# Kernel tuning notes

Hardware: AMD Instinct MI355X
Metric: run time of the kernel (lower is better)

Reference implementation:

```python
import jax, jax.numpy as jnp
import numpy as np

G = 256          # grid resolution -> V = G*G vertices
B = 8            # batch of meshes
N_SAMPLES = 2048
W_CHAMFER, W_EDGE, W_NORMAL, W_LAP = 1.0, 1.0, 0.1, 0.1
V = G * G


def _grid_faces(g):
    idx = np.arange(g * g).reshape(g, g)
    v00 = idx[:-1, :-1].ravel(); v01 = idx[:-1, 1:].ravel()
    v10 = idx[1:, :-1].ravel();  v11 = idx[1:, 1:].ravel()
    f1 = np.stack([v00, v01, v10], 1)
    f2 = np.stack([v01, v11, v10], 1)
    return np.concatenate([f1, f2], 0).astype(np.int32)  # [F,3]


def _edges_and_pairs(faces, n_verts):
    # all face-edge incidences + the opposite vertex of each incidence
    e = np.concatenate([faces[:, [0, 1]], faces[:, [1, 2]], faces[:, [0, 2]]], 0)
    opp = np.concatenate([faces[:, 2], faces[:, 0], faces[:, 1]], 0)
    e = np.sort(e, 1)
    key = e[:, 0].astype(np.int64) * n_verts + e[:, 1]
    order = np.argsort(key, kind='stable')
    key_s, es, opps = key[order], e[order], opp[order]
    first = np.ones(len(key_s), bool); first[1:] = key_s[1:] != key_s[:-1]
    edges = es[first].astype(np.int32)                      # unique undirected edges [E,2]
    dup = np.nonzero(~first)[0]                             # 2nd incidence of shared edges
    pairs = np.stack([es[dup - 1, 0], es[dup - 1, 1], opps[dup - 1], opps[dup]], 1).astype(np.int32)  # [P,4]
    return edges, pairs


def setup_inputs() -> dict:
    key = jax.random.key(0)
    faces = _grid_faces(G)
    edges, nc_pairs = _edges_and_pairs(faces, V)
    # base grid geometry + gaussian perturbation (realistic smooth-ish surfaces)
    xs, ys = np.meshgrid(np.linspace(0, 1, G), np.linspace(0, 1, G), indexing='ij')
    base = np.stack([xs, ys, 0.1 * np.sin(4 * np.pi * xs) * np.cos(4 * np.pi * ys)], -1).reshape(V, 3)
    k1, k2 = jax.random.split(key)
    verts_pred = jnp.asarray(base, jnp.float32)[None] + 0.01 * jax.random.normal(k1, (B, V, 3), jnp.float32)
    verts_targ = jnp.asarray(base, jnp.float32)[None] + 0.01 * jax.random.normal(k2, (B, V, 3), jnp.float32)
    return {
        'verts_pred': verts_pred,
        'verts_targ': verts_targ,
        'faces': jnp.asarray(faces),
        'edges': jnp.asarray(edges),
        'nc_pairs': jnp.asarray(nc_pairs),
    }


def _sample_points(verts, faces, key, n):
    # verts [V,3]; area-weighted face sampling + uniform barycentric (pytorch3d scheme)
    v0, v1, v2 = verts[faces[:, 0]], verts[faces[:, 1]], verts[faces[:, 2]]
    areas = 0.5 * jnp.linalg.norm(jnp.cross(v1 - v0, v2 - v0), axis=-1)          # [F]
    kf, kb = jax.random.split(key)
    fidx = jax.random.categorical(kf, jnp.log(areas + 1e-12), shape=(n,))        # [n]
    uv = jax.random.uniform(kb, (n, 2), verts.dtype)
    su = jnp.sqrt(uv[:, 0:1]); vv = uv[:, 1:2]
    w0, w1, w2 = 1.0 - su, su * (1.0 - vv), su * vv
    return w0 * v0[fidx] + w1 * v1[fidx] + w2 * v2[fidx]                         # [n,3]


def _chamfer(x, y):
    # squared-distance chamfer, mean over points then batch, both directions summed
    d = jnp.sum((x[:, :, None, :] - y[:, None, :, :]) ** 2, -1)                  # [B,N,M]
    return jnp.mean(jnp.min(d, axis=2)) + jnp.mean(jnp.min(d, axis=1))


def _edge_loss(verts, edges):
    diff = verts[:, edges[:, 0]] - verts[:, edges[:, 1]]                          # [B,E,3]
    return jnp.mean(jnp.sum(diff * diff, -1))                                     # (||e|| - 0)^2


def _normal_consistency(verts, nc_pairs):
    v0 = verts[:, nc_pairs[:, 0]]; v1 = verts[:, nc_pairs[:, 1]]
    a = verts[:, nc_pairs[:, 2]]; b = verts[:, nc_pairs[:, 3]]
    e = v1 - v0
    n0 = jnp.cross(e, a - v0)
    n1 = -jnp.cross(e, b - v0)
    eps = 1e-8
    cos = jnp.sum(n0 * n1, -1) / (
        jnp.maximum(jnp.linalg.norm(n0, axis=-1), eps)
        * jnp.maximum(jnp.linalg.norm(n1, axis=-1), eps))
    return jnp.mean(1.0 - cos)


def _laplacian_uniform(verts, edges):
    e0, e1 = edges[:, 0], edges[:, 1]
    ones = jnp.ones((edges.shape[0],), verts.dtype)

    def per_mesh(v):  # v [V,3]
        nsum = (jax.ops.segment_sum(v[e1], e0, num_segments=V)
                + jax.ops.segment_sum(v[e0], e1, num_segments=V))
        deg = (jax.ops.segment_sum(ones, e0, num_segments=V)
               + jax.ops.segment_sum(ones, e1, num_segments=V))
        lap = nsum / jnp.maximum(deg, 1.0)[:, None] - v                           # D^-1 A v - v
        return jnp.mean(jnp.linalg.norm(lap, axis=-1))

    return jnp.mean(jax.vmap(per_mesh)(verts))


def reference(verts_pred, verts_targ, faces, edges, nc_pairs):
    skey = jax.random.key(42)
    kp = jax.random.split(jax.random.fold_in(skey, 0), verts_pred.shape[0])
    kt = jax.random.split(jax.random.fold_in(skey, 1), verts_targ.shape[0])
    sample_pred = jax.vmap(lambda v, k: _sample_points(v, faces, k, N_SAMPLES))(verts_pred, kp)
    sample_targ = jax.vmap(lambda v, k: _sample_points(v, faces, k, N_SAMPLES))(verts_targ, kt)
    loss_chamfer = _chamfer(sample_pred, sample_targ)
    loss_edge = _edge_loss(verts_pred, edges)
    loss_normal = _normal_consistency(verts_pred, nc_pairs)
    loss_lap = _laplacian_uniform(verts_pred, edges)
    loss = (W_CHAMFER * loss_chamfer + W_EDGE * loss_edge
            + W_NORMAL * loss_normal + W_LAP * loss_lap)
    return (loss, loss_chamfer, loss_edge, loss_normal, loss_lap)
```

## Files before the change

kernel.cpp:

```cpp
#include <hip/hip_runtime.h>
#include <stdint.h>

#define GSZ 256
#define NV (GSZ*GSZ)
#define NS 2048
#define CELLS (255*255)
#define FH CELLS
#define NF (2*CELLS)
#define CH 8

struct F3 { float x, y, z; };

__device__ __forceinline__ F3 ldv3(const float* __restrict__ p, int idx) {
    const float* q = p + 3*(size_t)idx;
    F3 r; r.x = q[0]; r.y = q[1]; r.z = q[2]; return r;
}
__device__ __forceinline__ F3 f3sub(F3 a, F3 b) { return F3{a.x-b.x, a.y-b.y, a.z-b.z}; }
__device__ __forceinline__ F3 f3cross(F3 a, F3 b) {
    return F3{a.y*b.z - a.z*b.y, a.z*b.x - a.x*b.z, a.x*b.y - a.y*b.x};
}
__device__ __forceinline__ float f3dot(F3 a, F3 b) { return a.x*b.x + a.y*b.y + a.z*b.z; }

__device__ __forceinline__ uint64_t splitmix64(uint64_t& s) {
    s += 0x9E3779B97F4A7C15ULL;
    uint64_t z = s;
    z = (z ^ (z >> 30)) * 0xBF58476D1CE4E5B9ULL;
    z = (z ^ (z >> 27)) * 0x94D049BB133111EBULL;
    return z ^ (z >> 31);
}

__device__ __forceinline__ float blockReduceSum256(float v) {
    __shared__ float s[4];
    int lane = threadIdx.x & 63, w = threadIdx.x >> 6;
    #pragma unroll
    for (int o = 32; o > 0; o >>= 1) v += __shfl_down(v, o, 64);
    if (lane == 0) s[w] = v;
    __syncthreads();
    if (threadIdx.x == 0) v = s[0] + s[1] + s[2] + s[3];
    return v;
}

__global__ void k_area(const float* __restrict__ vp, const float* __restrict__ vt,
                       int B, float* __restrict__ areas, float* __restrict__ blockmax,
                       unsigned* __restrict__ counter) {
    if (blockIdx.x == 0 && threadIdx.x == 0) *counter = 0u;
    int gid = blockIdx.x*256 + threadIdx.x;
    int total = 2*B*CELLS;
    float mloc = 0.f;
    if (gid < total) {
        int m = gid / CELLS;
        int c = gid - m*CELLS;
        int i = c / 255, j = c - i*255;
        const float* verts = (m < B ? vp + (size_t)m*NV*3
                                    : vt + (size_t)(m-B)*NV*3);
        int b00 = i*GSZ + j;
        F3 v00 = ldv3(verts, b00);
        F3 v01 = ldv3(verts, b00+1);
        F3 v10 = ldv3(verts, b00+GSZ);
        F3 v11 = ldv3(verts, b00+GSZ+1);
        F3 c1 = f3cross(f3sub(v01, v00), f3sub(v10, v00));
        F3 c2 = f3cross(f3sub(v11, v01), f3sub(v10, v01));
        float a1 = 0.5f * sqrtf(f3dot(c1, c1));
        float a2 = 0.5f * sqrtf(f3dot(c2, c2));
        size_t base = (size_t)m*NF;
        areas[base + c]      = a1;
        areas[base + FH + c] = a2;
        mloc = fmaxf(a1, a2);
    }
    #pragma unroll
    for (int o = 32; o > 0; o >>= 1) mloc = fmaxf(mloc, __shfl_down(mloc, o, 64));
    __shared__ float s[4];
    int lane = threadIdx.x & 63, w = threadIdx.x >> 6;
    if (lane == 0) s[w] = mloc;
    __syncthreads();
    if (threadIdx.x == 0)
        blockmax[blockIdx.x] = fmaxf(fmaxf(s[0], s[1]), fmaxf(s[2], s[3]));
}

__global__ void k_sample(const float* __restrict__ vp, const float* __restrict__ vt,
                         int B, const float* __restrict__ areas,
                         const float* __restrict__ blockmax, int nbm,
                         float4* __restrict__ samples) {
    float m = 0.f;
    for (int k = threadIdx.x; k < nbm; k += 256) m = fmaxf(m, blockmax[k]);
    #pragma unroll
    for (int o = 32; o > 0; o >>= 1) m = fmaxf(m, __shfl_down(m, o, 64));
    __shared__ float s[4];
    int lane = threadIdx.x & 63, w = threadIdx.x >> 6;
    if (lane == 0) s[w] = m;
    __syncthreads();
    __shared__ float sMaxA;
    if (threadIdx.x == 0) sMaxA = fmaxf(fmaxf(s[0], s[1]), fmaxf(s[2], s[3]));
    __syncthreads();
    float maxA = sMaxA;

    int gid = blockIdx.x*256 + threadIdx.x;
    int cloud = gid / (B*NS);
    int rem = gid - cloud*(B*NS);
    int b = rem / NS;
    const float* verts = (cloud ? vt : vp) + (size_t)b*NV*3;
    const float* am = areas + (size_t)(cloud*B + b)*NF;

    uint64_t st = ((uint64_t)(gid + 1) * 0x9E3779B97F4A7C15ULL) ^ 0xC0FFEE123456789ULL;
    int f = 0;
    for (int round = 0; round < 64; ++round) {
        uint64_t r0 = splitmix64(st), r1 = splitmix64(st);
        uint64_t r2 = splitmix64(st), r3 = splitmix64(st);
        int f0 = (int)(((uint64_t)(uint32_t)r0 * (uint32_t)NF) >> 32);
        int f1 = (int)(((uint64_t)(uint32_t)r1 * (uint32_t)NF) >> 32);
        int f2 = (int)(((uint64_t)(uint32_t)r2 * (uint32_t)NF) >> 32);
        int f3 = (int)(((uint64_t)(uint32_t)r3 * (uint32_t)NF) >> 32);
        float a0 = am[f0], a1 = am[f1], a2 = am[f2], a3 = am[f3];
        float u0 = ((uint32_t)(r0 >> 40)) * (1.f/16777216.f);
        float u1 = ((uint32_t)(r1 >> 40)) * (1.f/16777216.f);
        float u2 = ((uint32_t)(r2 >> 40)) * (1.f/16777216.f);
        float u3 = ((uint32_t)(r3 >> 40)) * (1.f/16777216.f);
        if (u0 * maxA <= a0) { f = f0; break; }
        if (u1 * maxA <= a1) { f = f1; break; }
        if (u2 * maxA <= a2) { f = f2; break; }
        if (u3 * maxA <= a3) { f = f3; break; }
        f = f3;
    }
    int i0, i1, i2;
    if (f < FH) {
        int c = f;  int i = c / 255, j = c - i*255;  int v = i*GSZ + j;
        i0 = v; i1 = v + 1; i2 = v + GSZ;
    } else {
        int c = f - FH;  int i = c / 255, j = c - i*255;  int v = i*GSZ + j;
        i0 = v + 1; i1 = v + GSZ + 1; i2 = v + GSZ;
    }
    F3 v0 = ldv3(verts, i0), v1 = ldv3(verts, i1), v2 = ldv3(verts, i2);
    uint64_t r = splitmix64(st);
    float u0 = ((uint32_t)r >> 8) * (1.f/16777216.f);
    float u1 = ((uint32_t)(r >> 32) >> 8) * (1.f/16777216.f);
    float su = sqrtf(u0);
    float w0 = 1.f - su, w1 = su * (1.f - u1), w2 = su * u1;
    float X = w0*v0.x + w1*v1.x + w2*v2.x;
    float Y = w0*v0.y + w1*v1.y + w2*v2.y;
    float Z = w0*v0.z + w1*v1.z + w2*v2.z;
    samples[gid] = make_float4(X, Y, Z, X*X + Y*Y + Z*Z);
}

__global__ void k_heavy(const float* __restrict__ vp,
                        const float4* __restrict__ samples,
                        const int* __restrict__ edges, const int* __restrict__ ncp,
                        int B, int E, int P, int nbE, int nbP,
                        float* __restrict__ minpart,
                        float* __restrict__ partE, float* __restrict__ partP,
                        float* __restrict__ partV) {
    int bx = blockIdx.x, b = blockIdx.y;
    if (bx < 64) {
        int xh = bx >> 5, z = bx & 31;
        int dir = z >> 4, q = z & 15;
        const float4* src = samples + ((size_t)dir*B + b)*NS;
        const float4* dst = samples + ((size_t)(1-dir)*B + b)*NS;

        __shared__ float4 tile[128];
        if (threadIdx.x < 128) tile[threadIdx.x] = dst[q*128 + threadIdx.x];

        float nx[4], ny[4], nz[4], xx[4], mn[4];
        #pragma unroll
        for (int k = 0; k < 4; ++k) {
            int i = xh*1024 + k*256 + threadIdx.x;
            float4 sp = src[i];
            nx[k] = -2.f*sp.x; ny[k] = -2.f*sp.y; nz[k] = -2.f*sp.z;
            xx[k] = sp.w;
            mn[k] = 3.402823466e38f;
        }
        __syncthreads();
        #pragma unroll 4
        for (int j = 0; j < 128; ++j) {
            float4 t = tile[j];
            #pragma unroll
            for (int k = 0; k < 4; ++k) {
                float d = fmaf(nx[k], t.x, t.w);
                d = fmaf(ny[k], t.y, d);
                d = fmaf(nz[k], t.z, d);
                mn[k] = fminf(mn[k], d);
            }
        }
        float* outp = minpart + (((size_t)(dir*B + b)*16) + q)*NS;
        #pragma unroll
        for (int k = 0; k < 4; ++k)
            outp[xh*1024 + k*256 + threadIdx.x] = mn[k] + xx[k];
        return;
    }

    int mx = bx - 64;
    const float* verts = vp + (size_t)b*NV*3;
    float acc = 0.f;
    if (mx < nbE) {
        int base = mx*(256*CH);
        #pragma unroll 2
        for (int c = 0; c < CH; ++c) {
            int e = base + c*256 + threadIdx.x;
            if (e < E) {
                int2 ed = ((const int2*)edges)[e];
                F3 d = f3sub(ldv3(verts, ed.x), ldv3(verts, ed.y));
                acc += f3dot(d, d);
            }
        }
        float s = blockReduceSum256(acc);
        if (threadIdx.x == 0) partE[(size_t)mx*B + b] = s;
    } else if (mx < nbE + nbP) {
        int base = (mx - nbE)*(256*CH);
        for (int c = 0; c < CH; ++c) {
            int p = base + c*256 + threadIdx.x;
            if (p < P) {
                int4 q = ((const int4*)ncp)[p];
                F3 v0 = ldv3(verts, q.x), v1 = ldv3(verts, q.y);
                F3 a = ldv3(verts, q.z), bb = ldv3(verts, q.w);
                F3 e = f3sub(v1, v0);
                F3 n0 = f3cross(e, f3sub(a, v0));
                F3 n1 = f3cross(f3sub(bb, v0), e);
                float num = f3dot(n0, n1);
                float den2 = fmaxf(f3dot(n0, n0), 1e-16f) * fmaxf(f3dot(n1, n1), 1e-16f);
                acc += 1.f - num * rsqrtf(den2);
            }
        }
        float s = blockReduceSum256(acc);
        if (threadIdx.x == 0) partP[(size_t)(mx - nbE)*B + b] = s;
    } else {
        int base = (mx - nbE - nbP)*(256*CH);
        for (int c = 0; c < CH; ++c) {
            int idx = base + c*256 + threadIdx.x;
            int i = idx >> 8, j = idx & 255;
            F3 ctr = ldv3(verts, idx);
            float nx = 0.f, ny = 0.f, nz = 0.f; int deg = 0;
            #define ADDN(ii, jj) { F3 n_ = ldv3(verts, (ii)*GSZ + (jj)); \
                                   nx += n_.x; ny += n_.y; nz += n_.z; ++deg; }
            if (j > 0)               ADDN(i, j-1);
            if (j < GSZ-1)           ADDN(i, j+1);
            if (i > 0)               ADDN(i-1, j);
            if (i < GSZ-1)           ADDN(i+1, j);
            if (i < GSZ-1 && j > 0)  ADDN(i+1, j-1);
            if (i > 0 && j < GSZ-1)  ADDN(i-1, j+1);
            #undef ADDN
            float inv = 1.f / (float)deg;
            float lx = nx*inv - ctr.x, ly = ny*inv - ctr.y, lz = nz*inv - ctr.z;
            acc += sqrtf(lx*lx + ly*ly + lz*lz);
        }
        float s = blockReduceSum256(acc);
        if (threadIdx.x == 0) partV[(size_t)(mx - nbE - nbP)*B + b] = s;
    }
}

__global__ void k_redfin(const float* __restrict__ minpart, int B,
                         const float* __restrict__ partE, int nE,
                         const float* __restrict__ partP, int nP,
                         const float* __restrict__ partV, int nL,
                         int E, int P,
                         float* __restrict__ chamPart,
                         unsigned* __restrict__ counter,
                         float* __restrict__ out) {
    int gid = blockIdx.x*256 + threadIdx.x;
    int dir = gid / (B*NS);
    int rem = gid - dir*(B*NS);
    int b = rem / NS, i = rem - b*NS;
    const float* p = minpart + (size_t)(dir*B + b)*16*NS + i;
    float mn = 3.402823466e38f;
    #pragma unroll
    for (int q = 0; q < 16; ++q) mn = fminf(mn, p[(size_t)q*NS]);
    float sm = blockReduceSum256(mn);
    if (threadIdx.x == 0) chamPart[blockIdx.x] = sm;

    __shared__ unsigned sTicket;
    if (threadIdx.x == 0) {
        __threadfence();
        sTicket = atomicAdd(counter, 1u);
    }
    __syncthreads();
    if (sTicket != (unsigned)(gridDim.x - 1)) return;
    __threadfence();

    const volatile float* cp = chamPart;
    double a0 = 0, a1 = 0, aE = 0, aP = 0, aL = 0;
    for (int k = threadIdx.x; k < 64;  k += 256) a0 += (double)cp[k];
    for (int k = 64 + threadIdx.x; k < 128; k += 256) a1 += (double)cp[k];
    for (int k = threadIdx.x; k < nE; k += 256) aE += (double)partE[k];
    for (int k = threadIdx.x; k < nP; k += 256) aP += (double)partP[k];
    for (int k = threadIdx.x; k < nL; k += 256) aL += (double)partV[k];
    __shared__ double sd[5][4];
    double v[5] = {a0, a1, aE, aP, aL};
    int lane = threadIdx.x & 63, w = threadIdx.x >> 6;
    #pragma unroll
    for (int r = 0; r < 5; ++r) {
        double x = v[r];
        #pragma unroll
        for (int o = 32; o > 0; o >>= 1) x += __shfl_down(x, o, 64);
        if (lane == 0) sd[r][w] = x;
    }
    __syncthreads();
    if (threadIdx.x == 0) {
        double bn = (double)B * NS;
        double ch = (sd[0][0]+sd[0][1]+sd[0][2]+sd[0][3]) / bn
                  + (sd[1][0]+sd[1][1]+sd[1][2]+sd[1][3]) / bn;
        double ed = (sd[2][0]+sd[2][1]+sd[2][2]+sd[2][3]) / ((double)B * E);
        double no = (sd[3][0]+sd[3][1]+sd[3][2]+sd[3][3]) / ((double)B * P);
        double la = (sd[4][0]+sd[4][1]+sd[4][2]+sd[4][3]) / ((double)B * NV);
        double loss = ch + ed + 0.1*no + 0.1*la;
        out[0] = (float)loss; out[1] = (float)ch; out[2] = (float)ed;
        out[3] = (float)no;   out[4] = (float)la;
    }
}

extern "C" void kernel_launch(void* const* d_in, const int* in_sizes, int n_in,
                              void* d_out, int out_size, void* d_ws, size_t ws_size,
                              hipStream_t stream) {
    const float* vp = (const float*)d_in[0];
    const float* vt = (const float*)d_in[1];
    const int* edges = (const int*)d_in[3];
    const int* ncp   = (const int*)d_in[4];
    const int B = in_sizes[0] / (3*NV);
    const int E = in_sizes[3] / 2;
    const int P = in_sizes[4] / 4;

    char* ws = (char*)d_ws;
    size_t off = 0;
    auto alloc = [&](size_t bytes) -> void* {
        void* p = ws + off;
        off = (off + bytes + 255) & ~(size_t)255;
        return p;
    };
    float*    areas    = (float*)   alloc((size_t)2*B*NF*sizeof(float));
    float4*   samples  = (float4*)  alloc((size_t)2*B*NS*sizeof(float4));
    float*    minpart  = (float*)   alloc((size_t)2*B*16*NS*sizeof(float));
    float*    blockmax = (float*)   alloc(8192*sizeof(float));
    float*    chamPart = (float*)   alloc(256*sizeof(float));
    float*    partE    = (float*)   alloc(2048*sizeof(float));
    float*    partP    = (float*)   alloc(2048*sizeof(float));
    float*    partV    = (float*)   alloc(1024*sizeof(float));
    unsigned* counter  = (unsigned*)alloc(256);

    int nbm = (2*B*CELLS + 255)/256;
    k_area<<<nbm, 256, 0, stream>>>(vp, vt, B, areas, blockmax, counter);
    k_sample<<<(2*B*NS)/256, 256, 0, stream>>>(vp, vt, B, areas, blockmax, nbm, samples);
    int nbE = (E + 256*CH - 1)/(256*CH);
    int nbP = (P + 256*CH - 1)/(256*CH);
    int nbV = NV/(256*CH);
    dim3 gh(64 + nbE + nbP + nbV, B);
    k_heavy<<<gh, 256, 0, stream>>>(vp, samples, edges, ncp, B, E, P, nbE, nbP,
                                    minpart, partE, partP, partV);
    k_redfin<<<(2*B*NS)/256, 256, 0, stream>>>(minpart, B, partE, nbE*B,
                                               partP, nbP*B, partV, nbV*B,
                                               E, P, chamPart, counter,
                                               (float*)d_out);
}
```

Before: 144.1 us.

## Fuse point sampling into chamfer blocks and use atomic max for area

Removes the separate sampling kernel and the samples buffer. Each chamfer block now regenerates its source and destination points on the fly with the same deterministic RNG. The global max face area is found with an atomicMax on float bits into a control word, which a memset clears before launch, replacing the per-block max array and its re-reduction. This saves a kernel launch and a global round trip, but each sample is regenerated redundantly across many blocks: source points 16 times and tile points 2 times. The rejection-sampling loop with random gathers therefore repeats, lengthening the critical chamfer blocks.

```diff
diff --git a/kernel.cpp b/kernel.cpp
--- a/kernel.cpp
+++ b/kernel.cpp
@@ -40,10 +40,52 @@
     return v;
 }
 
+__device__ __forceinline__ float4 gen_sample(const float* __restrict__ verts,
+                                             const float* __restrict__ am,
+                                             float maxA, int gid) {
+    uint64_t st = ((uint64_t)(gid + 1) * 0x9E3779B97F4A7C15ULL) ^ 0xC0FFEE123456789ULL;
+    int f = 0;
+    for (int round = 0; round < 64; ++round) {
+        uint64_t r0 = splitmix64(st), r1 = splitmix64(st);
+        uint64_t r2 = splitmix64(st), r3 = splitmix64(st);
+        int f0 = (int)(((uint64_t)(uint32_t)r0 * (uint32_t)NF) >> 32);
+        int f1 = (int)(((uint64_t)(uint32_t)r1 * (uint32_t)NF) >> 32);
+        int f2 = (int)(((uint64_t)(uint32_t)r2 * (uint32_t)NF) >> 32);
+        int f3 = (int)(((uint64_t)(uint32_t)r3 * (uint32_t)NF) >> 32);
+        float a0 = am[f0], a1 = am[f1], a2 = am[f2], a3 = am[f3];
+        float u0 = ((uint32_t)(r0 >> 40)) * (1.f/16777216.f);
+        float u1 = ((uint32_t)(r1 >> 40)) * (1.f/16777216.f);
+        float u2 = ((uint32_t)(r2 >> 40)) * (1.f/16777216.f);
+        float u3 = ((uint32_t)(r3 >> 40)) * (1.f/16777216.f);
+        if (u0 * maxA <= a0) { f = f0; break; }
+        if (u1 * maxA <= a1) { f = f1; break; }
+        if (u2 * maxA <= a2) { f = f2; break; }
+        if (u3 * maxA <= a3) { f = f3; break; }
+        f = f3;
+    }
+    int i0, i1, i2;
+    if (f < FH) {
+        int c = f;  int i = c / 255, j = c - i*255;  int v = i*GSZ + j;
+        i0 = v; i1 = v + 1; i2 = v + GSZ;
+    } else {
+        int c = f - FH;  int i = c / 255, j = c - i*255;  int v = i*GSZ + j;
+        i0 = v + 1; i1 = v + GSZ + 1; i2 = v + GSZ;
+    }
+    F3 v0 = ldv3(verts, i0), v1 = ldv3(verts, i1), v2 = ldv3(verts, i2);
+    uint64_t r = splitmix64(st);
+    float u0 = ((uint32_t)r >> 8) * (1.f/16777216.f);
+    float u1 = ((uint32_t)(r >> 32) >> 8) * (1.f/16777216.f);
+    float su = sqrtf(u0);
+    float w0 = 1.f - su, w1 = su * (1.f - u1), w2 = su * u1;
+    float X = w0*v0.x + w1*v1.x + w2*v2.x;
+    float Y = w0*v0.y + w1*v1.y + w2*v2.y;
+    float Z = w0*v0.z + w1*v1.z + w2*v2.z;
+    return make_float4(X, Y, Z, X*X + Y*Y + Z*Z);
+}
+
 __global__ void k_area(const float* __restrict__ vp, const float* __restrict__ vt,
-                       int B, float* __restrict__ areas, float* __restrict__ blockmax,
-                       unsigned* __restrict__ counter) {
-    if (blockIdx.x == 0 && threadIdx.x == 0) *counter = 0u;
+                       int B, float* __restrict__ areas,
+                       unsigned* __restrict__ ctrl) {
     int gid = blockIdx.x*256 + threadIdx.x;
     int total = 2*B*CELLS;
     float mloc = 0.f;
@@ -73,76 +115,15 @@
     int lane = threadIdx.x & 63, w = threadIdx.x >> 6;
     if (lane == 0) s[w] = mloc;
     __syncthreads();
-    if (threadIdx.x == 0)
-        blockmax[blockIdx.x] = fmaxf(fmaxf(s[0], s[1]), fmaxf(s[2], s[3]));
-}
-
-__global__ void k_sample(const float* __restrict__ vp, const float* __restrict__ vt,
-                         int B, const float* __restrict__ areas,
-                         const float* __restrict__ blockmax, int nbm,
-                         float4* __restrict__ samples) {
-    float m = 0.f;
-    for (int k = threadIdx.x; k < nbm; k += 256) m = fmaxf(m, blockmax[k]);
-    #pragma unroll
-    for (int o = 32; o > 0; o >>= 1) m = fmaxf(m, __shfl_down(m, o, 64));
-    __shared__ float s[4];
-    int lane = threadIdx.x & 63, w = threadIdx.x >> 6;
-    if (lane == 0) s[w] = m;
-    __syncthreads();
-    __shared__ float sMaxA;
-    if (threadIdx.x == 0) sMaxA = fmaxf(fmaxf(s[0], s[1]), fmaxf(s[2], s[3]));
-    __syncthreads();
-    float maxA = sMaxA;
-
-    int gid = blockIdx.x*256 + threadIdx.x;
-    int cloud = gid / (B*NS);
-    int rem = gid - cloud*(B*NS);
-    int b = rem / NS;
-    const float* verts = (cloud ? vt : vp) + (size_t)b*NV*3;
-    const float* am = areas + (size_t)(cloud*B + b)*NF;
-
-    uint64_t st = ((uint64_t)(gid + 1) * 0x9E3779B97F4A7C15ULL) ^ 0xC0FFEE123456789ULL;
-    int f = 0;
-    for (int round = 0; round < 64; ++round) {
-        uint64_t r0 = splitmix64(st), r1 = splitmix64(st);
-        uint64_t r2 = splitmix64(st), r3 = splitmix64(st);
-        int f0 = (int)(((uint64_t)(uint32_t)r0 * (uint32_t)NF) >> 32);
-        int f1 = (int)(((uint64_t)(uint32_t)r1 * (uint32_t)NF) >> 32);
-        int f2 = (int)(((uint64_t)(uint32_t)r2 * (uint32_t)NF) >> 32);
-        int f3 = (int)(((uint64_t)(uint32_t)r3 * (uint32_t)NF) >> 32);
-        float a0 = am[f0], a1 = am[f1], a2 = am[f2], a3 = am[f3];
-        float u0 = ((uint32_t)(r0 >> 40)) * (1.f/16777216.f);
-        float u1 = ((uint32_t)(r1 >> 40)) * (1.f/16777216.f);
-        float u2 = ((uint32_t)(r2 >> 40)) * (1.f/16777216.f);
-        float u3 = ((uint32_t)(r3 >> 40)) * (1.f/16777216.f);
-        if (u0 * maxA <= a0) { f = f0; break; }
-        if (u1 * maxA <= a1) { f = f1; break; }
-        if (u2 * maxA <= a2) { f = f2; break; }
-        if (u3 * maxA <= a3) { f = f3; break; }
-        f = f3;
-    }
-    int i0, i1, i2;
-    if (f < FH) {
-        int c = f;  int i = c / 255, j = c - i*255;  int v = i*GSZ + j;
-        i0 = v; i1 = v + 1; i2 = v + GSZ;
-    } else {
-        int c = f - FH;  int i = c / 255, j = c - i*255;  int v = i*GSZ + j;
-        i0 = v + 1; i1 = v + GSZ + 1; i2 = v + GSZ;
-    }
-    F3 v0 = ldv3(verts, i0), v1 = ldv3(verts, i1), v2 = ldv3(verts, i2);
-    uint64_t r = splitmix64(st);
-    float u0 = ((uint32_t)r >> 8) * (1.f/16777216.f);
-    float u1 = ((uint32_t)(r >> 32) >> 8) * (1.f/16777216.f);
-    float su = sqrtf(u0);
-    float w0 = 1.f - su, w1 = su * (1.f - u1), w2 = su * u1;
-    float X = w0*v0.x + w1*v1.x + w2*v2.x;
-    float Y = w0*v0.y + w1*v1.y + w2*v2.y;
-    float Z = w0*v0.z + w1*v1.z + w2*v2.z;
-    samples[gid] = make_float4(X, Y, Z, X*X + Y*Y + Z*Z);
-}
-
-__global__ void k_heavy(const float* __restrict__ vp,
-                        const float4* __restrict__ samples,
+    if (threadIdx.x == 0) {
+        float blk = fmaxf(fmaxf(s[0], s[1]), fmaxf(s[2], s[3]));
+        atomicMax(&ctrl[1], __float_as_uint(blk));
+    }
+}
+
+__global__ void k_heavy(const float* __restrict__ vp, const float* __restrict__ vt,
+                        const float* __restrict__ areas,
+                        const unsigned* __restrict__ ctrl,
                         const int* __restrict__ edges, const int* __restrict__ ncp,
                         int B, int E, int P, int nbE, int nbP,
                         float* __restrict__ minpart,
@@ -152,17 +133,22 @@
     if (bx < 64) {
         int xh = bx >> 5, z = bx & 31;
         int dir = z >> 4, q = z & 15;
-        const float4* src = samples + ((size_t)dir*B + b)*NS;
-        const float4* dst = samples + ((size_t)(1-dir)*B + b)*NS;
+        const float* srcV = (dir ? vt : vp) + (size_t)b*NV*3;
+        const float* dstV = (dir ? vp : vt) + (size_t)b*NV*3;
+        const float* srcA = areas + (size_t)(dir*B + b)*NF;
+        const float* dstA = areas + (size_t)((1-dir)*B + b)*NF;
+        float maxA = __uint_as_float(ctrl[1]);
 
         __shared__ float4 tile[128];
-        if (threadIdx.x < 128) tile[threadIdx.x] = dst[q*128 + threadIdx.x];
-
+        if (threadIdx.x < 128) {
+            int dgid = ((1-dir)*B + b)*NS + q*128 + threadIdx.x;
+            tile[threadIdx.x] = gen_sample(dstV, dstA, maxA, dgid);
+        }
         float nx[4], ny[4], nz[4], xx[4], mn[4];
         #pragma unroll
         for (int k = 0; k < 4; ++k) {
-            int i = xh*1024 + k*256 + threadIdx.x;
-            float4 sp = src[i];
+            int sgid = (dir*B + b)*NS + xh*1024 + k*256 + threadIdx.x;
+            float4 sp = gen_sample(srcV, srcA, maxA, sgid);
             nx[k] = -2.f*sp.x; ny[k] = -2.f*sp.y; nz[k] = -2.f*sp.z;
             xx[k] = sp.w;
             mn[k] = 3.402823466e38f;
@@ -251,7 +237,7 @@
                          const float* __restrict__ partV, int nL,
                          int E, int P,
                          float* __restrict__ chamPart,
-                         unsigned* __restrict__ counter,
+                         unsigned* __restrict__ ctrl,
                          float* __restrict__ out) {
     int gid = blockIdx.x*256 + threadIdx.x;
     int dir = gid / (B*NS);
@@ -267,7 +253,7 @@
     __shared__ unsigned sTicket;
     if (threadIdx.x == 0) {
         __threadfence();
-        sTicket = atomicAdd(counter, 1u);
+        sTicket = atomicAdd(&ctrl[0], 1u);
     }
     __syncthreads();
     if (sTicket != (unsigned)(gridDim.x - 1)) return;
@@ -323,26 +309,26 @@
         return p;
     };
     float*    areas    = (float*)   alloc((size_t)2*B*NF*sizeof(float));
-    float4*   samples  = (float4*)  alloc((size_t)2*B*NS*sizeof(float4));
     float*    minpart  = (float*)   alloc((size_t)2*B*16*NS*sizeof(float));
-    float*    blockmax = (float*)   alloc(8192*sizeof(float));
     float*    chamPart = (float*)   alloc(256*sizeof(float));
     float*    partE    = (float*)   alloc(2048*sizeof(float));
     float*    partP    = (float*)   alloc(2048*sizeof(float));
     float*    partV    = (float*)   alloc(1024*sizeof(float));
-    unsigned* counter  = (unsigned*)alloc(256);
+    unsigned* ctrl     = (unsigned*)alloc(256);
+
+    hipMemsetAsync(ctrl, 0, 8, stream);
 
     int nbm = (2*B*CELLS + 255)/256;
-    k_area<<<nbm, 256, 0, stream>>>(vp, vt, B, areas, blockmax, counter);
-    k_sample<<<(2*B*NS)/256, 256, 0, stream>>>(vp, vt, B, areas, blockmax, nbm, samples);
+    k_area<<<nbm, 256, 0, stream>>>(vp, vt, B, areas, ctrl);
     int nbE = (E + 256*CH - 1)/(256*CH);
     int nbP = (P + 256*CH - 1)/(256*CH);
     int nbV = NV/(256*CH);
     dim3 gh(64 + nbE + nbP + nbV, B);
-    k_heavy<<<gh, 256, 0, stream>>>(vp, samples, edges, ncp, B, E, P, nbE, nbP,
+    k_heavy<<<gh, 256, 0, stream>>>(vp, vt, areas, ctrl, edges, ncp,
+                                    B, E, P, nbE, nbP,
                                     minpart, partE, partP, partV);
     k_redfin<<<(2*B*NS)/256, 256, 0, stream>>>(minpart, B, partE, nbE*B,
                                                partP, nbP*B, partV, nbV*B,
-                                               E, P, chamPart, counter,
+                                               E, P, chamPart, ctrl,
                                                (float*)d_out);
 }
```

New measurement: 236.9 us. 64.4% more time.
